# Kernel optimization log

Measured on AMD Instinct MI355X. Metric: run time of the kernel, lower is better.

Reference implementation:

```python
import jax, jax.numpy as jnp
import numpy as np
from jax import lax

T = 2048          # tokens (batch*seq, module flattens to [-1, hidden])
H = 2048          # hidden_size
E = 32            # n_routed_experts
DF = 1024         # moe_intermediate_size
DS = 4096         # moe_shared_expert_intermediate_size
TOP_K = 6         # num_experts_per_tok
N_GROUP = 8
TOPK_GROUP = 4
SCALE = 2.5       # routed_scaling_factor
NORM_TOPK = True


def relu2(x):
    r = jax.nn.relu(x)
    return r * r


def setup_inputs() -> dict:
    key = jax.random.key(0)
    ks = jax.random.split(key, 7)
    s = 0.02
    return {
        "x": jax.random.normal(ks[0], (T, H), dtype=jnp.float32),
        "router_w": jax.random.normal(ks[1], (E, H), dtype=jnp.float32) * s,
        "router_b": jax.random.normal(ks[2], (E,), dtype=jnp.float32) * s,
        "w_up": jax.random.normal(ks[3], (E, H, DF), dtype=jnp.float32) * s,
        "w_down": jax.random.normal(ks[4], (E, DF, H), dtype=jnp.float32) * s,
        "shared_up": jax.random.normal(ks[5], (H, DS), dtype=jnp.float32) * s,
        "shared_down": jax.random.normal(ks[6], (DS, H), dtype=jnp.float32) * s,
    }


def _route(x, router_w, router_b):
    # router in fp32: logits -> sigmoid scores -> group-restricted top-k
    logits = x @ router_w.T                                  # [T, E]
    scores = jax.nn.sigmoid(logits)
    sfc = scores + router_b[None, :]                         # scores_for_choice
    gsize = E // N_GROUP
    grp = sfc.reshape(T, N_GROUP, gsize)
    group_scores = lax.top_k(grp, 2)[0].sum(-1)              # [T, n_group] sum of top-2
    _, gidx = lax.top_k(group_scores, TOPK_GROUP)            # [T, topk_group]
    group_mask = jax.nn.one_hot(gidx, N_GROUP, dtype=sfc.dtype).sum(1)  # [T, n_group]
    score_mask = jnp.repeat(group_mask, gsize, axis=1)       # [T, E]
    masked = jnp.where(score_mask > 0, sfc, 0.0)
    _, tidx = lax.top_k(masked, TOP_K)                       # [T, top_k]
    tw = jnp.take_along_axis(scores, tidx, axis=1)           # gather raw scores
    if NORM_TOPK:
        tw = tw / (tw.sum(-1, keepdims=True) + 1e-20)
    tw = tw * SCALE
    return tidx, tw


def reference(x, router_w, router_b, w_up, w_down, shared_up, shared_down):
    tidx, tw = _route(x, router_w, router_b)
    # dense combine weights [T, E]; equals sum of routed weights per expert
    combine = (jax.nn.one_hot(tidx, E, dtype=tw.dtype) * tw[..., None]).sum(1)
    # routed experts (no bias, so scaling before down_proj == scaling the output)
    h = jnp.einsum('td,edf->tef', x, w_up)                   # [T, E, DF]
    a = relu2(h) * combine[:, :, None]
    moe_out = jnp.einsum('tef,efd->td', a, w_down)           # [T, H]
    shared_out = relu2(x @ shared_up) @ shared_down
    return moe_out + shared_out
```

## Files before the change

kernel.cpp:

```cpp
#include <hip/hip_runtime.h>
#include <hip/hip_bf16.h>
#include <math.h>

#define T_TOK 2048
#define HID   2048
#define NE    32
#define DF    1024
#define DSZ   4096
#define TOPK  6
#define NGRP  8
#define TOPKG 4
#define RSCALE 2.5f

typedef __attribute__((ext_vector_type(8))) short short8;
typedef __attribute__((ext_vector_type(4))) float f32x4;

static __device__ __forceinline__ unsigned short f2b(float f) {
    union { float f; unsigned u; } v; v.f = f;
    unsigned r = v.u + 0x7fffu + ((v.u >> 16) & 1u);
    return (unsigned short)(r >> 16);
}

__global__ void router_kernel(const float* __restrict__ x,
                              const float* __restrict__ rw,
                              const float* __restrict__ rb,
                              int* __restrict__ tidx, float* __restrict__ tw,
                              int* __restrict__ counts) {
    __shared__ float xs[HID];
    __shared__ float part[256];
    __shared__ float scores[NE];
    __shared__ float sfc[NE];
    int t = blockIdx.x;
    int tid = threadIdx.x;
    for (int i = tid; i < HID / 4; i += 256) {
        ((float4*)xs)[i] = ((const float4*)(x + (size_t)t * HID))[i];
    }
    __syncthreads();
    int e = tid & 31, ch = tid >> 5;
    const float* w = rw + (size_t)e * HID + ch * 256;
    const float* xv = xs + ch * 256;
    float p = 0.f;
    #pragma unroll 8
    for (int k = 0; k < 256; ++k) p += xv[k] * w[k];
    part[tid] = p;
    __syncthreads();
    if (tid < 32) {
        float l = 0.f;
        #pragma unroll
        for (int c = 0; c < 8; ++c) l += part[c * 32 + tid];
        float s = 1.f / (1.f + expf(-l));
        scores[tid] = s;
        sfc[tid] = s + rb[tid];
    }
    __syncthreads();
    if (tid == 0) {
        float gs[NGRP];
        for (int g = 0; g < NGRP; ++g) {
            float v[4];
            for (int i = 0; i < 4; ++i) v[i] = sfc[g * 4 + i];
            int bi = 0;
            for (int i = 1; i < 4; ++i) if (v[i] > v[bi]) bi = i;
            float m1 = v[bi]; v[bi] = -INFINITY;
            int bj = 0;
            for (int i = 1; i < 4; ++i) if (v[i] > v[bj]) bj = i;
            gs[g] = m1 + v[bj];
        }
        bool gsel[NGRP];
        for (int g = 0; g < NGRP; ++g) gsel[g] = false;
        for (int k = 0; k < TOPKG; ++k) {
            int bi = -1; float b = -INFINITY;
            for (int g = 0; g < NGRP; ++g)
                if (!gsel[g] && gs[g] > b) { b = gs[g]; bi = g; }
            gsel[bi] = true;
        }
        float masked[NE];
        for (int i = 0; i < NE; ++i) masked[i] = gsel[i >> 2] ? sfc[i] : 0.0f;
        int sel[TOPK]; float wv[TOPK]; float wsum = 0.f;
        for (int k = 0; k < TOPK; ++k) {
            int bi = -1; float b = -INFINITY;
            for (int i = 0; i < NE; ++i)
                if (masked[i] > b) { b = masked[i]; bi = i; }
            masked[bi] = -INFINITY;
            sel[k] = bi; wv[k] = scores[bi]; wsum += wv[k];
        }
        float inv = RSCALE / (wsum + 1e-20f);
        for (int k = 0; k < TOPK; ++k) {
            tidx[t * TOPK + k] = sel[k];
            tw[t * TOPK + k] = wv[k] * inv;
            atomicAdd(&counts[sel[k]], 1);
        }
    }
}

__global__ void scan_kernel(const int* __restrict__ counts, int* __restrict__ offsets) {
    if (threadIdx.x == 0) {
        int a = 0;
        for (int e2 = 0; e2 < NE; ++e2) { offsets[e2] = a; a += counts[e2]; }
        offsets[NE] = a;
    }
}

__global__ void scatter_kernel(const int* __restrict__ tidx, const float* __restrict__ tw,
                               const int* __restrict__ offsets, int* __restrict__ cursors,
                               int* __restrict__ perm, float* __restrict__ pw) {
    int t = blockIdx.x * blockDim.x + threadIdx.x;
    if (t >= T_TOK) return;
    for (int k = 0; k < TOPK; ++k) {
        int e = tidx[t * TOPK + k];
        int pos = atomicAdd(&cursors[e], 1);
        int slot = offsets[e] + pos;
        perm[slot] = t;
        pw[slot] = tw[t * TOPK + k];
    }
}

__global__ void cvt_x_kernel(const float* __restrict__ src, unsigned short* __restrict__ dst, int n8) {
    int i = blockIdx.x * blockDim.x + threadIdx.x;
    if (i >= n8) return;
    float4 a = ((const float4*)src)[i * 2];
    float4 b = ((const float4*)src)[i * 2 + 1];
    short8 o;
    o[0] = (short)f2b(a.x); o[1] = (short)f2b(a.y); o[2] = (short)f2b(a.z); o[3] = (short)f2b(a.w);
    o[4] = (short)f2b(b.x); o[5] = (short)f2b(b.y); o[6] = (short)f2b(b.z); o[7] = (short)f2b(b.w);
    *(short8*)(dst + (size_t)i * 8) = o;
}

__global__ void transpose_bf16_kernel(const float* __restrict__ src, unsigned short* __restrict__ dst,
                                      int K, int N) {
    __shared__ unsigned short tile[64][72];
    size_t mat = blockIdx.z;
    src += mat * (size_t)K * N;
    dst += mat * (size_t)K * N;
    int k0 = blockIdx.y * 64, n0 = blockIdx.x * 64;
    int tid = threadIdx.x;
    int r = tid >> 4, c4 = (tid & 15) * 4;
    #pragma unroll
    for (int p = 0; p < 4; ++p) {
        int kk = r + p * 16;
        float4 v = *(const float4*)(src + (size_t)(k0 + kk) * N + n0 + c4);
        tile[c4 + 0][kk] = f2b(v.x);
        tile[c4 + 1][kk] = f2b(v.y);
        tile[c4 + 2][kk] = f2b(v.z);
        tile[c4 + 3][kk] = f2b(v.w);
    }
    __syncthreads();
    int nr = tid >> 3, kc = (tid & 7) * 8;
    #pragma unroll
    for (int p = 0; p < 2; ++p) {
        int nn = nr + p * 32;
        short8 o;
        #pragma unroll
        for (int i = 0; i < 8; ++i) o[i] = tile[nn][kc + i];
        *(short8*)(dst + (size_t)(n0 + nn) * K + k0 + kc) = o;
    }
}

template<int MODE, int AB16, int BT>
__global__ __launch_bounds__(256, 2)
void gemm_kernel(const void* __restrict__ Ain, const void* __restrict__ Bin,
                 void* __restrict__ Cout, const int* __restrict__ offsets,
                 const int* __restrict__ perm, const float* __restrict__ pw,
                 float* __restrict__ outbuf) {
    constexpr int K = (MODE == 0 || MODE == 2) ? HID : (MODE == 1 ? DSZ : DF);
    constexpr int N = (MODE == 0) ? DSZ : (MODE == 2 ? DF : HID);
    constexpr bool GATH = (MODE == 2);

    __shared__ __align__(16) char lds[32768];
    char* As = lds;
    char* Bs = lds + 16384;

    int tid = threadIdx.x;
    int lane = tid & 63, wvid = tid >> 6, wr = wvid >> 1, wc = wvid & 1;

    int row0, rowEnd;
    int e = 0;
    if (MODE == 2 || MODE == 3) {
        e = blockIdx.z;
        int off = offsets[e], end = offsets[e + 1];
        row0 = off + blockIdx.y * 128;
        if (row0 >= end) return;
        rowEnd = end;
    } else {
        row0 = blockIdx.y * 128;
        rowEnd = 1 << 30;
    }
    int n0 = blockIdx.x * 128;

    int sr = tid >> 3;
    int sc = tid & 7;
    size_t asrc[4];
    #pragma unroll
    for (int p = 0; p < 4; ++p) {
        int gr = row0 + p * 32 + sr;
        if ((MODE == 2 || MODE == 3) && gr > rowEnd - 1) gr = rowEnd - 1;
        int s = GATH ? perm[gr] : gr;
        asrc[p] = (size_t)s * K;
    }
    int bcol = tid & 127;
    int bkh = tid >> 7;

    f32x4 acc[4][4] = {};

    for (int k0 = 0; k0 < K; k0 += 64) {
        __syncthreads();
        #pragma unroll
        for (int p = 0; p < 4; ++p) {
            int r = p * 32 + sr;
            short8 av;
            if (AB16) {
                av = *(const short8*)((const unsigned short*)Ain + asrc[p] + k0 + sc * 8);
            } else {
                const float* src = (const float*)Ain + asrc[p] + k0 + sc * 8;
                float4 v0 = *(const float4*)(src);
                float4 v1 = *(const float4*)(src + 4);
                av[0] = (short)f2b(v0.x); av[1] = (short)f2b(v0.y);
                av[2] = (short)f2b(v0.z); av[3] = (short)f2b(v0.w);
                av[4] = (short)f2b(v1.x); av[5] = (short)f2b(v1.y);
                av[6] = (short)f2b(v1.z); av[7] = (short)f2b(v1.w);
            }
            *(short8*)(As + r * 128 + ((sc * 16) ^ ((r & 7) << 4))) = av;
        }
        if (BT) {
            const unsigned short* Btb = (const unsigned short*)Bin + (size_t)e * N * K;
            #pragma unroll
            for (int p = 0; p < 4; ++p) {
                int r = p * 32 + sr;
                short8 bv = *(const short8*)(Btb + (size_t)(n0 + r) * K + k0 + sc * 8);
                *(short8*)(Bs + r * 128 + ((sc * 16) ^ ((r & 7) << 4))) = bv;
            }
        } else {
            const float* B = (const float*)Bin + (size_t)e * (size_t)K * N;
            const float* bs = B + (size_t)(k0 + bkh * 32) * N + (n0 + bcol);
            short8 bv[4];
            #pragma unroll
            for (int q = 0; q < 4; ++q)
                #pragma unroll
                for (int i = 0; i < 8; ++i)
                    bv[q][i] = (short)f2b(bs[(size_t)(q * 8 + i) * N]);
            int swz = (bcol & 7) << 4;
            #pragma unroll
            for (int q = 0; q < 4; ++q)
                *(short8*)(Bs + bcol * 128 + ((bkh * 64 + q * 16) ^ swz)) = bv[q];
        }
        __syncthreads();
        #pragma unroll
        for (int ks = 0; ks < 2; ++ks) {
            int kg = lane >> 4, r16 = lane & 15;
            short8 af[4], bfr[4];
            #pragma unroll
            for (int m = 0; m < 4; ++m) {
                int r = wr * 64 + m * 16 + r16;
                af[m] = *(const short8*)(As + r * 128 + ((ks * 64 + kg * 16) ^ ((r & 7) << 4)));
            }
            #pragma unroll
            for (int n = 0; n < 4; ++n) {
                int c = wc * 64 + n * 16 + r16;
                bfr[n] = *(const short8*)(Bs + c * 128 + ((ks * 64 + kg * 16) ^ ((c & 7) << 4)));
            }
            #pragma unroll
            for (int m = 0; m < 4; ++m)
                #pragma unroll
                for (int n = 0; n < 4; ++n)
                    acc[m][n] = __builtin_amdgcn_mfma_f32_16x16x32_bf16(af[m], bfr[n], acc[m][n], 0, 0, 0);
        }
    }

    int r16 = lane & 15, rg = lane >> 4;
    #pragma unroll
    for (int m = 0; m < 4; ++m) {
        #pragma unroll
        for (int j = 0; j < 4; ++j) {
            int rr = row0 + wr * 64 + m * 16 + rg * 4 + j;
            if (MODE == 0) {
                unsigned short* Cb = (unsigned short*)Cout;
                #pragma unroll
                for (int n = 0; n < 4; ++n) {
                    int cc = n0 + wc * 64 + n * 16 + r16;
                    float v = acc[m][n][j];
                    v = v > 0.f ? v * v : 0.f;
                    Cb[(size_t)rr * N + cc] = f2b(v);
                }
            } else if (MODE == 2) {
                if (rr < rowEnd) {
                    unsigned short* Cb = (unsigned short*)Cout;
                    float scale = pw[rr];
                    #pragma unroll
                    for (int n = 0; n < 4; ++n) {
                        int cc = n0 + wc * 64 + n * 16 + r16;
                        float v = acc[m][n][j];
                        v = v > 0.f ? v * v : 0.f;
                        Cb[(size_t)rr * N + cc] = f2b(v * scale);
                    }
                }
            } else if (MODE == 1) {
                float* Cf = (float*)Cout;
                #pragma unroll
                for (int n = 0; n < 4; ++n) {
                    int cc = n0 + wc * 64 + n * 16 + r16;
                    Cf[(size_t)rr * N + cc] = acc[m][n][j];
                }
            } else {
                if (rr < rowEnd) {
                    int tok = perm[rr];
                    #pragma unroll
                    for (int n = 0; n < 4; ++n) {
                        int cc = n0 + wc * 64 + n * 16 + r16;
                        unsafeAtomicAdd(&outbuf[(size_t)tok * HID + cc], acc[m][n][j]);
                    }
                }
            }
        }
    }
}

extern "C" void kernel_launch(void* const* d_in, const int* in_sizes, int n_in,
                              void* d_out, int out_size, void* d_ws, size_t ws_size,
                              hipStream_t stream) {
    const float* x     = (const float*)d_in[0];
    const float* rw    = (const float*)d_in[1];
    const float* rb    = (const float*)d_in[2];
    const float* w_up  = (const float*)d_in[3];
    const float* w_dn  = (const float*)d_in[4];
    const float* sh_up = (const float*)d_in[5];
    const float* sh_dn = (const float*)d_in[6];
    float* out = (float*)d_out;
    char* ws = (char*)d_ws;

    int*   counts  = (int*)(ws);
    int*   cursors = (int*)(ws + 128);
    int*   offsets = (int*)(ws + 256);
    int*   tidx    = (int*)(ws + 1024);
    float* tw      = (float*)(ws + 1024 + 49152);
    int*   perm    = (int*)(ws + 102400);
    float* pw      = (float*)(ws + 102400 + 49152);
    unsigned short* act   = (unsigned short*)(ws + 204800);
    unsigned short* shact = (unsigned short*)(ws + 204800 + 25165824);
    unsigned short* xb    = (unsigned short*)(ws + 204800 + 25165824 + 16777216);
    const size_t base_end = 204800ull + 25165824ull + 16777216ull + 8388608ull;
    unsigned short* buf   = (unsigned short*)(ws + base_end);

    int lvl;
    if (ws_size < base_end) lvl = 0;
    else if (ws_size >= base_end + 134217728ull) lvl = 3;
    else if (ws_size >= base_end + 16777216ull) lvl = 2;
    else lvl = 1;

    hipMemsetAsync(ws, 0, 256, stream);
    router_kernel<<<T_TOK, 256, 0, stream>>>(x, rw, rb, tidx, tw, counts);
    scan_kernel<<<1, 64, 0, stream>>>(counts, offsets);
    scatter_kernel<<<(T_TOK + 255) / 256, 256, 0, stream>>>(tidx, tw, offsets, cursors, perm, pw);
    if (lvl >= 1) cvt_x_kernel<<<T_TOK * HID / 8 / 256, 256, 0, stream>>>(x, xb, T_TOK * HID / 8);

    dim3 gridS0(DSZ / 128, T_TOK / 128);
    dim3 gridS1(HID / 128, T_TOK / 128);
    dim3 gridR2(DF / 128, T_TOK / 128, NE);
    dim3 gridR3(HID / 128, T_TOK / 128, NE);

    if (lvl >= 2) {
        transpose_bf16_kernel<<<dim3(DSZ / 64, HID / 64, 1), 256, 0, stream>>>(sh_up, buf, HID, DSZ);
        gemm_kernel<0, 1, 1><<<gridS0, 256, 0, stream>>>(xb, buf, shact, nullptr, nullptr, nullptr, nullptr);
    } else if (lvl == 1) {
        gemm_kernel<0, 1, 0><<<gridS0, 256, 0, stream>>>(xb, sh_up, shact, nullptr, nullptr, nullptr, nullptr);
    } else {
        gemm_kernel<0, 0, 0><<<gridS0, 256, 0, stream>>>(x, sh_up, shact, nullptr, nullptr, nullptr, nullptr);
    }
    if (lvl >= 2) {
        transpose_bf16_kernel<<<dim3(HID / 64, DSZ / 64, 1), 256, 0, stream>>>(sh_dn, buf, DSZ, HID);
        gemm_kernel<1, 1, 1><<<gridS1, 256, 0, stream>>>(shact, buf, out, nullptr, nullptr, nullptr, nullptr);
    } else {
        gemm_kernel<1, 1, 0><<<gridS1, 256, 0, stream>>>(shact, sh_dn, out, nullptr, nullptr, nullptr, nullptr);
    }
    if (lvl >= 3) {
        transpose_bf16_kernel<<<dim3(DF / 64, HID / 64, NE), 256, 0, stream>>>(w_up, buf, HID, DF);
        gemm_kernel<2, 1, 1><<<gridR2, 256, 0, stream>>>(xb, buf, act, offsets, perm, pw, nullptr);
    } else if (lvl >= 1) {
        gemm_kernel<2, 1, 0><<<gridR2, 256, 0, stream>>>(xb, w_up, act, offsets, perm, pw, nullptr);
    } else {
        gemm_kernel<2, 0, 0><<<gridR2, 256, 0, stream>>>(x, w_up, act, offsets, perm, pw, nullptr);
    }
    if (lvl >= 3) {
        transpose_bf16_kernel<<<dim3(HID / 64, DF / 64, NE), 256, 0, stream>>>(w_dn, buf, DF, HID);
        gemm_kernel<3, 1, 1><<<gridR3, 256, 0, stream>>>(act, buf, nullptr, offsets, perm, pw, out);
    } else {
        gemm_kernel<3, 1, 0><<<gridR3, 256, 0, stream>>>(act, w_dn, nullptr, offsets, perm, pw, out);
    }
}
```

Measured before the change: 646.9 us.

## Use direct global-to-LDS loads, fuse x conversion into router, replace atomics with slot combine

GEMM tile loads on the pre-transposed bf16 paths now use global_load_lds to copy 16-byte chunks straight into shared memory with an XOR-swizzled source column, skipping the register round trip. The separate x-to-bf16 conversion kernel is folded into the router, which already stages each token row in LDS. When the workspace is large enough, the routed down-projection writes per-slot outputs to a buffer, and a combine kernel sums the top-k slots per token instead of doing float atomics into the output. This costs an extra ~100MB buffer write and read plus one more launch, in exchange for removing atomic contention.

```diff
diff --git a/kernel.cpp b/kernel.cpp
--- a/kernel.cpp
+++ b/kernel.cpp
@@ -15,6 +15,13 @@
 typedef __attribute__((ext_vector_type(8))) short short8;
 typedef __attribute__((ext_vector_type(4))) float f32x4;
 
+typedef __attribute__((address_space(1))) const void gv1;
+typedef __attribute__((address_space(3))) void lv3;
+
+static __device__ __forceinline__ void gload16(const void* g, void* l) {
+    __builtin_amdgcn_global_load_lds((gv1*)g, (lv3*)l, 16, 0, 0);
+}
+
 static __device__ __forceinline__ unsigned short f2b(float f) {
     union { float f; unsigned u; } v; v.f = f;
     unsigned r = v.u + 0x7fffu + ((v.u >> 16) & 1u);
@@ -25,7 +32,8 @@
                               const float* __restrict__ rw,
                               const float* __restrict__ rb,
                               int* __restrict__ tidx, float* __restrict__ tw,
-                              int* __restrict__ counts) {
+                              int* __restrict__ counts,
+                              unsigned short* __restrict__ xb) {
     __shared__ float xs[HID];
     __shared__ float part[256];
     __shared__ float scores[NE];
@@ -36,6 +44,14 @@
         ((float4*)xs)[i] = ((const float4*)(x + (size_t)t * HID))[i];
     }
     __syncthreads();
+    if (xb) {
+        float4 a = ((const float4*)xs)[tid * 2];
+        float4 b = ((const float4*)xs)[tid * 2 + 1];
+        short8 o;
+        o[0] = (short)f2b(a.x); o[1] = (short)f2b(a.y); o[2] = (short)f2b(a.z); o[3] = (short)f2b(a.w);
+        o[4] = (short)f2b(b.x); o[5] = (short)f2b(b.y); o[6] = (short)f2b(b.z); o[7] = (short)f2b(b.w);
+        *(short8*)(xb + (size_t)t * HID + tid * 8) = o;
+    }
     int e = tid & 31, ch = tid >> 5;
     const float* w = rw + (size_t)e * HID + ch * 256;
     const float* xv = xs + ch * 256;
@@ -102,7 +118,8 @@
 
 __global__ void scatter_kernel(const int* __restrict__ tidx, const float* __restrict__ tw,
                                const int* __restrict__ offsets, int* __restrict__ cursors,
-                               int* __restrict__ perm, float* __restrict__ pw) {
+                               int* __restrict__ perm, float* __restrict__ pw,
+                               int* __restrict__ slot_of) {
     int t = blockIdx.x * blockDim.x + threadIdx.x;
     if (t >= T_TOK) return;
     for (int k = 0; k < TOPK; ++k) {
@@ -111,6 +128,7 @@
         int slot = offsets[e] + pos;
         perm[slot] = t;
         pw[slot] = tw[t * TOPK + k];
+        slot_of[t * TOPK + k] = slot;
     }
 }
 
@@ -155,7 +173,26 @@
     }
 }
 
-template<int MODE, int AB16, int BT>
+__global__ void combine_kernel(const float* __restrict__ slotout, const int* __restrict__ slot_of,
+                               float* __restrict__ out) {
+    int t = blockIdx.x, tid = threadIdx.x;
+    int s[TOPK];
+    #pragma unroll
+    for (int k = 0; k < TOPK; ++k) s[k] = slot_of[t * TOPK + k];
+    #pragma unroll
+    for (int p = 0; p < 2; ++p) {
+        int c = (p * 256 + tid) * 4;
+        float4 a = *(const float4*)(out + (size_t)t * HID + c);
+        #pragma unroll
+        for (int k = 0; k < TOPK; ++k) {
+            float4 v = *(const float4*)(slotout + (size_t)s[k] * HID + c);
+            a.x += v.x; a.y += v.y; a.z += v.z; a.w += v.w;
+        }
+        *(float4*)(out + (size_t)t * HID + c) = a;
+    }
+}
+
+template<int MODE, int AB16, int BT, int GL, int SLOT>
 __global__ __launch_bounds__(256, 2)
 void gemm_kernel(const void* __restrict__ Ain, const void* __restrict__ Bin,
                  void* __restrict__ Cout, const int* __restrict__ offsets,
@@ -186,61 +223,88 @@
     }
     int n0 = blockIdx.x * 128;
 
-    int sr = tid >> 3;
-    int sc = tid & 7;
+    int lr = lane >> 3;
+    int csrc = (((lane & 7) ^ lr) << 4);
+    size_t abyte[4], bbyte[4];
+    int ldsoff[4];
+    int sr = tid >> 3, sc = tid & 7;
     size_t asrc[4];
-    #pragma unroll
-    for (int p = 0; p < 4; ++p) {
-        int gr = row0 + p * 32 + sr;
-        if ((MODE == 2 || MODE == 3) && gr > rowEnd - 1) gr = rowEnd - 1;
-        int s = GATH ? perm[gr] : gr;
-        asrc[p] = (size_t)s * K;
+    if (GL) {
+        #pragma unroll
+        for (int p = 0; p < 4; ++p) {
+            int r = p * 32 + wvid * 8 + lr;
+            int gr = row0 + r;
+            if ((MODE == 2 || MODE == 3) && gr > rowEnd - 1) gr = rowEnd - 1;
+            int s = GATH ? perm[gr] : gr;
+            abyte[p] = (size_t)s * (K * 2);
+            bbyte[p] = (size_t)(n0 + r) * (K * 2);
+            ldsoff[p] = (p * 32 + wvid * 8) * 128;
+        }
+    } else {
+        #pragma unroll
+        for (int p = 0; p < 4; ++p) {
+            int gr = row0 + p * 32 + sr;
+            if ((MODE == 2 || MODE == 3) && gr > rowEnd - 1) gr = rowEnd - 1;
+            int s = GATH ? perm[gr] : gr;
+            asrc[p] = (size_t)s * K;
+        }
     }
     int bcol = tid & 127;
     int bkh = tid >> 7;
 
+    const char* Ab = (const char*)Ain;
+    const char* Bb = (const char*)Bin + (size_t)e * ((size_t)N * K * 2);
+
     f32x4 acc[4][4] = {};
 
     for (int k0 = 0; k0 < K; k0 += 64) {
         __syncthreads();
-        #pragma unroll
-        for (int p = 0; p < 4; ++p) {
-            int r = p * 32 + sr;
-            short8 av;
-            if (AB16) {
-                av = *(const short8*)((const unsigned short*)Ain + asrc[p] + k0 + sc * 8);
-            } else {
-                const float* src = (const float*)Ain + asrc[p] + k0 + sc * 8;
-                float4 v0 = *(const float4*)(src);
-                float4 v1 = *(const float4*)(src + 4);
-                av[0] = (short)f2b(v0.x); av[1] = (short)f2b(v0.y);
-                av[2] = (short)f2b(v0.z); av[3] = (short)f2b(v0.w);
-                av[4] = (short)f2b(v1.x); av[5] = (short)f2b(v1.y);
-                av[6] = (short)f2b(v1.z); av[7] = (short)f2b(v1.w);
-            }
-            *(short8*)(As + r * 128 + ((sc * 16) ^ ((r & 7) << 4))) = av;
-        }
-        if (BT) {
-            const unsigned short* Btb = (const unsigned short*)Bin + (size_t)e * N * K;
+        if (GL) {
+            #pragma unroll
+            for (int p = 0; p < 4; ++p) {
+                gload16(Ab + abyte[p] + k0 * 2 + csrc, As + ldsoff[p]);
+                gload16(Bb + bbyte[p] + k0 * 2 + csrc, Bs + ldsoff[p]);
+            }
+        } else {
             #pragma unroll
             for (int p = 0; p < 4; ++p) {
                 int r = p * 32 + sr;
-                short8 bv = *(const short8*)(Btb + (size_t)(n0 + r) * K + k0 + sc * 8);
-                *(short8*)(Bs + r * 128 + ((sc * 16) ^ ((r & 7) << 4))) = bv;
-            }
-        } else {
-            const float* B = (const float*)Bin + (size_t)e * (size_t)K * N;
-            const float* bs = B + (size_t)(k0 + bkh * 32) * N + (n0 + bcol);
-            short8 bv[4];
-            #pragma unroll
-            for (int q = 0; q < 4; ++q)
-                #pragma unroll
-                for (int i = 0; i < 8; ++i)
-                    bv[q][i] = (short)f2b(bs[(size_t)(q * 8 + i) * N]);
-            int swz = (bcol & 7) << 4;
-            #pragma unroll
-            for (int q = 0; q < 4; ++q)
-                *(short8*)(Bs + bcol * 128 + ((bkh * 64 + q * 16) ^ swz)) = bv[q];
+                short8 av;
+                if (AB16) {
+                    av = *(const short8*)((const unsigned short*)Ain + asrc[p] + k0 + sc * 8);
+                } else {
+                    const float* src = (const float*)Ain + asrc[p] + k0 + sc * 8;
+                    float4 v0 = *(const float4*)(src);
+                    float4 v1 = *(const float4*)(src + 4);
+                    av[0] = (short)f2b(v0.x); av[1] = (short)f2b(v0.y);
+                    av[2] = (short)f2b(v0.z); av[3] = (short)f2b(v0.w);
+                    av[4] = (short)f2b(v1.x); av[5] = (short)f2b(v1.y);
+                    av[6] = (short)f2b(v1.z); av[7] = (short)f2b(v1.w);
+                }
+                *(short8*)(As + r * 128 + ((sc * 16) ^ ((r & 7) << 4))) = av;
+            }
+            if (BT) {
+                const unsigned short* Btb = (const unsigned short*)Bin + (size_t)e * N * K;
+                #pragma unroll
+                for (int p = 0; p < 4; ++p) {
+                    int r = p * 32 + sr;
+                    short8 bv = *(const short8*)(Btb + (size_t)(n0 + r) * K + k0 + sc * 8);
+                    *(short8*)(Bs + r * 128 + ((sc * 16) ^ ((r & 7) << 4))) = bv;
+                }
+            } else {
+                const float* B = (const float*)Bin + (size_t)e * (size_t)K * N;
+                const float* bs = B + (size_t)(k0 + bkh * 32) * N + (n0 + bcol);
+                short8 bv[4];
+                #pragma unroll
+                for (int q = 0; q < 4; ++q)
+                    #pragma unroll
+                    for (int i = 0; i < 8; ++i)
+                        bv[q][i] = (short)f2b(bs[(size_t)(q * 8 + i) * N]);
+                int swz = (bcol & 7) << 4;
+                #pragma unroll
+                for (int q = 0; q < 4; ++q)
+                    *(short8*)(Bs + bcol * 128 + ((bkh * 64 + q * 16) ^ swz)) = bv[q];
+            }
         }
         __syncthreads();
         #pragma unroll
@@ -301,11 +365,20 @@
                 }
             } else {
                 if (rr < rowEnd) {
-                    int tok = perm[rr];
-                    #pragma unroll
-                    for (int n = 0; n < 4; ++n) {
-                        int cc = n0 + wc * 64 + n * 16 + r16;
-                        unsafeAtomicAdd(&outbuf[(size_t)tok * HID + cc], acc[m][n][j]);
+                    if (SLOT) {
+                        float* Cf = (float*)Cout;
+                        #pragma unroll
+                        for (int n = 0; n < 4; ++n) {
+                            int cc = n0 + wc * 64 + n * 16 + r16;
+                            Cf[(size_t)rr * N + cc] = acc[m][n][j];
+                        }
+                    } else {
+                        int tok = perm[rr];
+                        #pragma unroll
+                        for (int n = 0; n < 4; ++n) {
+                            int cc = n0 + wc * 64 + n * 16 + r16;
+                            unsafeAtomicAdd(&outbuf[(size_t)tok * HID + cc], acc[m][n][j]);
+                        }
                     }
                 }
             }
@@ -330,26 +403,30 @@
     int*   cursors = (int*)(ws + 128);
     int*   offsets = (int*)(ws + 256);
     int*   tidx    = (int*)(ws + 1024);
-    float* tw      = (float*)(ws + 1024 + 49152);
+    float* tw      = (float*)(ws + 50176);
     int*   perm    = (int*)(ws + 102400);
-    float* pw      = (float*)(ws + 102400 + 49152);
-    unsigned short* act   = (unsigned short*)(ws + 204800);
-    unsigned short* shact = (unsigned short*)(ws + 204800 + 25165824);
-    unsigned short* xb    = (unsigned short*)(ws + 204800 + 25165824 + 16777216);
-    const size_t base_end = 204800ull + 25165824ull + 16777216ull + 8388608ull;
+    float* pw      = (float*)(ws + 151552);
+    int*   slot_of = (int*)(ws + 200704);
+    unsigned short* act   = (unsigned short*)(ws + 249856);
+    unsigned short* shact = (unsigned short*)(ws + 25415680);
+    unsigned short* xb    = (unsigned short*)(ws + 42192896);
+    const size_t base_end = 50581504ull;
     unsigned short* buf   = (unsigned short*)(ws + base_end);
+    const size_t buf_end  = base_end + 134217728ull;
+    float* slotout = (float*)(ws + buf_end);
+    const size_t slot_end = buf_end + 100663296ull;
 
     int lvl;
     if (ws_size < base_end) lvl = 0;
-    else if (ws_size >= base_end + 134217728ull) lvl = 3;
-    else if (ws_size >= base_end + 16777216ull) lvl = 2;
+    else if (ws_size >= buf_end) lvl = 3;
+    else if (ws_size >= base_end + 33554432ull) lvl = 2;
     else lvl = 1;
+    bool use_slot = (lvl >= 3) && (ws_size >= slot_end);
 
     hipMemsetAsync(ws, 0, 256, stream);
-    router_kernel<<<T_TOK, 256, 0, stream>>>(x, rw, rb, tidx, tw, counts);
+    router_kernel<<<T_TOK, 256, 0, stream>>>(x, rw, rb, tidx, tw, counts, lvl >= 1 ? xb : nullptr);
     scan_kernel<<<1, 64, 0, stream>>>(counts, offsets);
-    scatter_kernel<<<(T_TOK + 255) / 256, 256, 0, stream>>>(tidx, tw, offsets, cursors, perm, pw);
-    if (lvl >= 1) cvt_x_kernel<<<T_TOK * HID / 8 / 256, 256, 0, stream>>>(x, xb, T_TOK * HID / 8);
+    scatter_kernel<<<(T_TOK + 255) / 256, 256, 0, stream>>>(tidx, tw, offsets, cursors, perm, pw, slot_of);
 
     dim3 gridS0(DSZ / 128, T_TOK / 128);
     dim3 gridS1(HID / 128, T_TOK / 128);
@@ -358,30 +435,35 @@
 
     if (lvl >= 2) {
         transpose_bf16_kernel<<<dim3(DSZ / 64, HID / 64, 1), 256, 0, stream>>>(sh_up, buf, HID, DSZ);
-        gemm_kernel<0, 1, 1><<<gridS0, 256, 0, stream>>>(xb, buf, shact, nullptr, nullptr, nullptr, nullptr);
+        gemm_kernel<0, 1, 1, 1, 0><<<gridS0, 256, 0, stream>>>(xb, buf, shact, nullptr, nullptr, nullptr, nullptr);
     } else if (lvl == 1) {
-        gemm_kernel<0, 1, 0><<<gridS0, 256, 0, stream>>>(xb, sh_up, shact, nullptr, nullptr, nullptr, nullptr);
-    } else {
-        gemm_kernel<0, 0, 0><<<gridS0, 256, 0, stream>>>(x, sh_up, shact, nullptr, nullptr, nullptr, nullptr);
+        gemm_kernel<0, 1, 0, 0, 0><<<gridS0, 256, 0, stream>>>(xb, sh_up, shact, nullptr, nullptr, nullptr, nullptr);
+    } else {
+        gemm_kernel<0, 0, 0, 0, 0><<<gridS0, 256, 0, stream>>>(x, sh_up, shact, nullptr, nullptr, nullptr, nullptr);
     }
     if (lvl >= 2) {
         transpose_bf16_kernel<<<dim3(HID / 64, DSZ / 64, 1), 256, 0, stream>>>(sh_dn, buf, DSZ, HID);
-        gemm_kernel<1, 1, 1><<<gridS1, 256, 0, stream>>>(shact, buf, out, nullptr, nullptr, nullptr, nullptr);
-    } else {
-        gemm_kernel<1, 1, 0><<<gridS1, 256, 0, stream>>>(shact, sh_dn, out, nullptr, nullptr, nullptr, nullptr);
+        gemm_kernel<1, 1, 1, 1, 0><<<gridS1, 256, 0, stream>>>(shact, buf, out, nullptr, nullptr, nullptr, nullptr);
+    } else {
+        gemm_kernel<1, 1, 0, 0, 0><<<gridS1, 256, 0, stream>>>(shact, sh_dn, out, nullptr, nullptr, nullptr, nullptr);
     }
     if (lvl >= 3) {
         transpose_bf16_kernel<<<dim3(DF / 64, HID / 64, NE), 256, 0, stream>>>(w_up, buf, HID, DF);
-        gemm_kernel<2, 1, 1><<<gridR2, 256, 0, stream>>>(xb, buf, act, offsets, perm, pw, nullptr);
+        gemm_kernel<2, 1, 1, 1, 0><<<gridR2, 256, 0, stream>>>(xb, buf, act, offsets, perm, pw, nullptr);
     } else if (lvl >= 1) {
-        gemm_kernel<2, 1, 0><<<gridR2, 256, 0, stream>>>(xb, w_up, act, offsets, perm, pw, nullptr);
-    } else {
-        gemm_kernel<2, 0, 0><<<gridR2, 256, 0, stream>>>(x, w_up, act, offsets, perm, pw, nullptr);
+        gemm_kernel<2, 1, 0, 0, 0><<<gridR2, 256, 0, stream>>>(xb, w_up, act, offsets, perm, pw, nullptr);
+    } else {
+        gemm_kernel<2, 0, 0, 0, 0><<<gridR2, 256, 0, stream>>>(x, w_up, act, offsets, perm, pw, nullptr);
     }
     if (lvl >= 3) {
         transpose_bf16_kernel<<<dim3(HID / 64, DF / 64, NE), 256, 0, stream>>>(w_dn, buf, DF, HID);
-        gemm_kernel<3, 1, 1><<<gridR3, 256, 0, stream>>>(act, buf, nullptr, offsets, perm, pw, out);
-    } else {
-        gemm_kernel<3, 1, 0><<<gridR3, 256, 0, stream>>>(act, w_dn, nullptr, offsets, perm, pw, out);
-    }
-}
+        if (use_slot) {
+            gemm_kernel<3, 1, 1, 1, 1><<<gridR3, 256, 0, stream>>>(act, buf, slotout, offsets, perm, pw, nullptr);
+            combine_kernel<<<T_TOK, 256, 0, stream>>>(slotout, slot_of, out);
+        } else {
+            gemm_kernel<3, 1, 1, 1, 0><<<gridR3, 256, 0, stream>>>(act, buf, nullptr, offsets, perm, pw, out);
+        }
+    } else {
+        gemm_kernel<3, 1, 0, 0, 0><<<gridR3, 256, 0, stream>>>(act, w_dn, nullptr, offsets, perm, pw, out);
+    }
+}
```

After: 628.0 us. -2.9%, faster.
